# Kernel tuning notes

Measured on AMD Instinct MI355X. Metric: run time of the kernel, lower is better.

The kernel has to match this reference:

```python
import jax, jax.numpy as jnp
import numpy as np

N_USERS = 100000
N_ITEMS = 50000
DIM = 64
RANK = 5
NNZ = 2000000
GNN_LAYER = 2
MODEL_CAT_RATE = 0.02  # args.model_cat_rate
TEMP = 0.2


def _l2norm(x):
    # torch F.normalize(p=2, dim=1, eps=1e-12)
    n = jnp.sqrt(jnp.sum(x * x, axis=1, keepdims=True))
    return x / jnp.maximum(n, 1e-12)


def setup_inputs() -> dict:
    key = jax.random.key(0)
    ks = jax.random.split(key, 16)
    s = 0.1
    inp = {
        "user_emb": jax.random.normal(ks[0], (N_USERS, DIM), jnp.float32) * s,
        "item_emb": jax.random.normal(ks[1], (N_ITEMS, DIM), jnp.float32) * s,
        "user_emb_pre": jax.random.normal(ks[2], (N_USERS, DIM), jnp.float32) * s,
        "item_emb_pre": jax.random.normal(ks[3], (N_ITEMS, DIM), jnp.float32) * s,
        "image_item_embeds": jax.random.normal(ks[4], (N_ITEMS, DIM), jnp.float32),
        "text_item_embeds": jax.random.normal(ks[5], (N_ITEMS, DIM), jnp.float32),
        "image_user_embeds": jax.random.normal(ks[6], (N_USERS, DIM), jnp.float32),
        "text_user_embeds": jax.random.normal(ks[7], (N_USERS, DIM), jnp.float32),
        "adj_rows": jax.random.randint(ks[8], (NNZ,), 0, N_USERS, jnp.int32),
        "adj_cols": jax.random.randint(ks[9], (NNZ,), 0, N_ITEMS, jnp.int32),
        "adj_vals": jax.random.uniform(ks[10], (NNZ,), jnp.float32) * 0.05,
        "ut": jax.random.normal(ks[11], (RANK, N_USERS), jnp.float32) * 0.01,
        "vt": jax.random.normal(ks[12], (RANK, N_ITEMS), jnp.float32) * 0.01,
        "u_mul_s": jax.random.normal(ks[13], (N_USERS, RANK), jnp.float32) * 0.01,
        "v_mul_s": jax.random.normal(ks[14], (N_ITEMS, RANK), jnp.float32) * 0.01,
        "uids": jax.random.randint(ks[15], (2048,), 0, N_USERS, jnp.int32),
        "iids": jax.random.randint(jax.random.fold_in(key, 99), (4096,), 0, N_ITEMS, jnp.int32),
    }
    return inp


def reference(user_emb, item_emb, user_emb_pre, item_emb_pre,
              image_item_embeds, text_item_embeds,
              image_user_embeds, text_user_embeds,
              adj_rows, adj_cols, adj_vals,
              ut, vt, u_mul_s, v_mul_s, uids, iids):
    Eu0 = user_emb_pre + user_emb  # [N_U, D]
    Ei0 = item_emb_pre + item_emb  # [N_I, D]

    E_u_list, E_i_list = [Eu0], [Ei0]
    G_u_list, G_i_list = [Eu0], [Ei0]
    for _ in range(GNN_LAYER):
        Ei_prev, Eu_prev = E_i_list[-1], E_u_list[-1]
        # sparse adj_norm @ E_i  and  adj_norm.T @ E_u (COO gather + segment_sum)
        Zu = jax.ops.segment_sum(adj_vals[:, None] * Ei_prev[adj_cols], adj_rows,
                                 num_segments=N_USERS)
        Zi = jax.ops.segment_sum(adj_vals[:, None] * Eu_prev[adj_rows], adj_cols,
                                 num_segments=N_ITEMS)
        # low-rank SVD propagation
        Gu = u_mul_s @ (vt @ Ei_prev)  # [N_U, D]
        Gi = v_mul_s @ (ut @ Eu_prev)  # [N_I, D]
        E_u_list.append(Zu); E_i_list.append(Zi)
        G_u_list.append(Gu); G_i_list.append(Gi)

    G_u = sum(G_u_list) / len(G_u_list)
    G_i = sum(G_i_list) / len(G_i_list)
    E_u = sum(E_u_list) / len(E_u_list)
    E_i = sum(E_i_list) / len(E_i_list)

    # contrastive InfoNCE-style loss
    neg = jax.nn.logsumexp((G_u[uids] @ E_u.T) / TEMP, axis=1).mean()
    neg = neg + jax.nn.logsumexp((G_i[iids] @ E_i.T) / TEMP, axis=1).mean()
    pos = jnp.clip(jnp.sum(G_u[uids] * E_u[uids], axis=1) / TEMP, -5.0, 5.0).mean()
    pos = pos + jnp.clip(jnp.sum(G_i[iids] * E_i[iids], axis=1) / TEMP, -5.0, 5.0).mean()
    gcl_loss = (-pos + neg) * (len(G_u_list) + 1)

    user_out = E_u + MODEL_CAT_RATE * _l2norm(image_user_embeds) \
                   + MODEL_CAT_RATE * _l2norm(text_user_embeds)
    item_out = E_i + MODEL_CAT_RATE * _l2norm(image_item_embeds) \
                   + MODEL_CAT_RATE * _l2norm(text_item_embeds)
    return user_out, item_out, gcl_loss
```

## Files before the change

kernel.cpp:

```cpp
#include <hip/hip_runtime.h>
#include <cstdint>

#define N_U 100000
#define N_I 50000
#define DIM 64
#define RANK 5
#define NNZ_ 2000000
#define M_U 2048
#define M_I 4096
#define NSEG 150000
#define BSH 8
#define NBUCK 586
#define NPB 512
#define CH 3907

#define CPC 3136
#define CPW 784
#define NCH_U 32
#define NCH_I 16
#define NPAD_U (CPC * NCH_U)
#define NPAD_I (CPC * NCH_I)

typedef __attribute__((ext_vector_type(8))) short short8;
typedef __attribute__((ext_vector_type(4))) float floatx4;

static constexpr size_t ZU1 = 0;
static constexpr size_t ZI1 = 6400000;
static constexpr size_t EDGE = 9600000;
static constexpr size_t P_OFF = 13600000;
static constexpr size_t Q_OFF = 13600320;
static constexpr size_t ACC_OFF = 13600640;
static constexpr size_t CNT_OFF = 13600704;
static constexpr size_t OFF_OFF = 13750704;
static constexpr size_t BCNT_OFF = 13900720;
static constexpr size_t BOFF_OFF = 13910144;
static constexpr size_t BSUM_OFF = 13919552;
static constexpr size_t EU0 = 13920576;
static constexpr size_t EI0 = EU0 + 6400000;
static constexpr size_t PART_U = EI0 + 3200000;
static constexpr size_t PART_I = PART_U + (size_t)M_U * NCH_U * 4;
static constexpr size_t GTU = PART_I + (size_t)M_I * NCH_I * 4;
static constexpr size_t GTI = GTU + 3200000;
static constexpr size_t STAGE_SV = 0;
static constexpr size_t BH_OFF = EDGE;
static constexpr size_t BHP_OFF = EDGE + (size_t)NPB * NBUCK;
static constexpr size_t EBU16 = 0;
static constexpr size_t EBI16 = 3211264;
static constexpr size_t GBU16 = EBI16 + 1605632;
static constexpr size_t GBI16 = GBU16 + 65536;

static __device__ __forceinline__ short f2bf(float x) {
    unsigned u = __builtin_bit_cast(unsigned, x);
    unsigned r = (u + 0x7fffu + ((u >> 16) & 1u)) >> 16;
    return (short)r;
}

static __device__ __forceinline__ float bfu(unsigned short u) {
    return __builtin_bit_cast(float, (unsigned)u << 16);
}

static __device__ __forceinline__ float vdec(unsigned p) {
    return __builtin_bit_cast(float, (p & 0x7FFFu) << 16);
}

__global__ void ew_add_kernel(const float4* __restrict__ a, const float4* __restrict__ b,
                              float4* __restrict__ o, int n) {
    int i = blockIdx.x * blockDim.x + threadIdx.x;
    if (i < n) {
        float4 x = a[i], y = b[i];
        o[i] = make_float4(x.x + y.x, x.y + y.y, x.z + y.z, x.w + y.w);
    }
}

__global__ __launch_bounds__(256) void bhist_kernel(const int* __restrict__ rows,
                                                    const int* __restrict__ cols,
                                                    int* __restrict__ bh) {
    __shared__ int h[NBUCK];
    for (int i = threadIdx.x; i < NBUCK; i += 256) h[i] = 0;
    __syncthreads();
    int b = blockIdx.x;
    int lo = b * CH, hi = min(lo + CH, NNZ_);
    for (int e = lo + threadIdx.x; e < hi; e += 256) {
        atomicAdd(&h[rows[e] >> BSH], 1);
        atomicAdd(&h[(N_U + cols[e]) >> BSH], 1);
    }
    __syncthreads();
    for (int i = threadIdx.x; i < NBUCK; i += 256) bh[(size_t)b * NBUCK + i] = h[i];
}

__global__ __launch_bounds__(256) void col_scan_kernel(const int* __restrict__ bh,
                                                       int* __restrict__ bhp,
                                                       int* __restrict__ bcnt) {
    int j = blockIdx.x * 256 + threadIdx.x;
    if (j >= NBUCK) return;
    int run = 0;
#pragma unroll 16
    for (int b = 0; b < NPB; b++) {
        int v = bh[(size_t)b * NBUCK + j];
        bhp[(size_t)b * NBUCK + j] = run;
        run += v;
    }
    bcnt[j] = run;
}

__global__ void scan1_kernel(const int* __restrict__ cnt, int* __restrict__ bsum, int n) {
    int i = blockIdx.x * 256 + threadIdx.x;
    int v = (i < n) ? cnt[i] : 0;
#pragma unroll
    for (int off = 32; off; off >>= 1) v += __shfl_down(v, off);
    __shared__ int ls[4];
    int lane = threadIdx.x & 63, w = threadIdx.x >> 6;
    if (lane == 0) ls[w] = v;
    __syncthreads();
    if (threadIdx.x == 0) bsum[blockIdx.x] = ls[0] + ls[1] + ls[2] + ls[3];
}

__global__ void scan2_kernel(int* __restrict__ bsum, int nb) {
    __shared__ int s[1024];
    int t = threadIdx.x;
    s[t] = (t < nb) ? bsum[t] : 0;
    __syncthreads();
    for (int off = 1; off < 1024; off <<= 1) {
        int v = (t >= off) ? s[t - off] : 0;
        __syncthreads();
        s[t] += v;
        __syncthreads();
    }
    if (t < nb) bsum[t] = (t == 0) ? 0 : s[t - 1];
}

__global__ void scan3_kernel(const int* __restrict__ cnt, const int* __restrict__ bsum,
                             int* __restrict__ off, int n) {
    __shared__ int s[256];
    int i = blockIdx.x * 256 + threadIdx.x;
    int t = threadIdx.x;
    int c = (i < n) ? cnt[i] : 0;
    s[t] = c;
    __syncthreads();
    for (int o = 1; o < 256; o <<= 1) {
        int v = (t >= o) ? s[t - o] : 0;
        __syncthreads();
        s[t] += v;
        __syncthreads();
    }
    if (i < n) off[i] = bsum[blockIdx.x] + s[t] - c;
}

__global__ __launch_bounds__(256) void bucket_place_kernel(
    const int* __restrict__ rows, const int* __restrict__ cols, const float* __restrict__ vals,
    const int* __restrict__ boff, const int* __restrict__ bhp, float2* __restrict__ sv) {
    __shared__ int h[NBUCK];
    for (int i = threadIdx.x; i < NBUCK; i += 256) h[i] = 0;
    __syncthreads();
    int b = blockIdx.x;
    int lo = b * CH, hi = min(lo + CH, NNZ_);
    const int* bhpb = bhp + (size_t)b * NBUCK;
    for (int e = lo + threadIdx.x; e < hi; e += 256) {
        int r = rows[e], c = cols[e];
        float v = vals[e];
        int bu = r >> BSH;
        int ru = atomicAdd(&h[bu], 1);
        sv[boff[bu] + bhpb[bu] + ru] = make_float2(__int_as_float(c | ((r & 255) << 20)), v);
        int sI = N_U + c;
        int bi = sI >> BSH;
        int ri = atomicAdd(&h[bi], 1);
        sv[boff[bi] + bhpb[bi] + ri] = make_float2(__int_as_float(r | ((sI & 255) << 20)), v);
    }
}

__global__ __launch_bounds__(256) void place2_kernel(const float2* __restrict__ sv,
                                                     const int* __restrict__ boff,
                                                     const int* __restrict__ bcnt,
                                                     int* __restrict__ off, int* __restrict__ cnt,
                                                     unsigned* __restrict__ edge) {
    int b = blockIdx.x;
    int start = boff[b], n = bcnt[b];
    __shared__ int h[256], hs[256], hc[256];
    h[threadIdx.x] = 0;
    hc[threadIdx.x] = 0;
    __syncthreads();
    for (int i = start + threadIdx.x; i < start + n; i += 256) {
        int packed = __float_as_int(sv[i].x);
        atomicAdd(&h[(packed >> 20) & 255], 1);
    }
    __syncthreads();
    if (threadIdx.x == 0) {
        int run = 0;
#pragma unroll
        for (int k = 0; k < 256; k++) { hs[k] = run; run += h[k]; }
    }
    __syncthreads();
    {
        int seg = b * 256 + threadIdx.x;
        if (seg < NSEG) {
            cnt[seg] = h[threadIdx.x];
            off[seg] = start + hs[threadIdx.x] + h[threadIdx.x];
        }
    }
    for (int i = start + threadIdx.x; i < start + n; i += 256) {
        float2 p = sv[i];
        int packed = __float_as_int(p.x);
        int s = (packed >> 20) & 255;
        int r = atomicAdd(&hc[s], 1);
        unsigned vb = (unsigned)(unsigned short)f2bf(p.y);
        edge[start + hs[s] + r] = ((unsigned)(packed & 0xFFFFF) << 15) | (vb & 0x7FFFu);
    }
}

__global__ __launch_bounds__(256) void spmm_csr_kernel(
    const unsigned* __restrict__ edge, const int* __restrict__ off, const int* __restrict__ cnt,
    int base, const unsigned short* __restrict__ E16, float* __restrict__ out, float scale,
    int accum, int nrows) {
    int lane = threadIdx.x & 63;
    int row = (blockIdx.x * blockDim.x + threadIdx.x) >> 6;
    if (row >= nrows) return;
    int end = off[base + row];
    int n = cnt[base + row];
    int e = end - n;
    float acc = 0.f;
    while (e < end) {
        int m = min(64, end - e);
        unsigned pk = (lane < m) ? edge[e + lane] : 0u;
        int j = 0;
        for (; j + 8 <= m; j += 8) {
            unsigned p0 = (unsigned)__builtin_amdgcn_readlane((int)pk, j + 0);
            unsigned p1 = (unsigned)__builtin_amdgcn_readlane((int)pk, j + 1);
            unsigned p2 = (unsigned)__builtin_amdgcn_readlane((int)pk, j + 2);
            unsigned p3 = (unsigned)__builtin_amdgcn_readlane((int)pk, j + 3);
            unsigned p4 = (unsigned)__builtin_amdgcn_readlane((int)pk, j + 4);
            unsigned p5 = (unsigned)__builtin_amdgcn_readlane((int)pk, j + 5);
            unsigned p6 = (unsigned)__builtin_amdgcn_readlane((int)pk, j + 6);
            unsigned p7 = (unsigned)__builtin_amdgcn_readlane((int)pk, j + 7);
            float g0 = bfu(E16[(size_t)(p0 >> 15) * 64 + lane]);
            float g1 = bfu(E16[(size_t)(p1 >> 15) * 64 + lane]);
            float g2 = bfu(E16[(size_t)(p2 >> 15) * 64 + lane]);
            float g3 = bfu(E16[(size_t)(p3 >> 15) * 64 + lane]);
            float g4 = bfu(E16[(size_t)(p4 >> 15) * 64 + lane]);
            float g5 = bfu(E16[(size_t)(p5 >> 15) * 64 + lane]);
            float g6 = bfu(E16[(size_t)(p6 >> 15) * 64 + lane]);
            float g7 = bfu(E16[(size_t)(p7 >> 15) * 64 + lane]);
            acc = __builtin_fmaf(vdec(p0), g0, acc);
            acc = __builtin_fmaf(vdec(p1), g1, acc);
            acc = __builtin_fmaf(vdec(p2), g2, acc);
            acc = __builtin_fmaf(vdec(p3), g3, acc);
            acc = __builtin_fmaf(vdec(p4), g4, acc);
            acc = __builtin_fmaf(vdec(p5), g5, acc);
            acc = __builtin_fmaf(vdec(p6), g6, acc);
            acc = __builtin_fmaf(vdec(p7), g7, acc);
        }
        for (; j < m; j++) {
            unsigned p = (unsigned)__builtin_amdgcn_readlane((int)pk, j);
            acc = __builtin_fmaf(vdec(p), bfu(E16[(size_t)(p >> 15) * 64 + lane]), acc);
        }
        e += m;
    }
    size_t o = (size_t)row * 64 + lane;
    if (accum) out[o] += scale * acc;
    else out[o] = acc;
}

__global__ __launch_bounds__(256) void rank_kernel(const float* __restrict__ X,
                                                   const float* __restrict__ W,
                                                   float* __restrict__ P, int n) {
    int lane = threadIdx.x & 63;
    int g = lane >> 4;
    int t = lane & 15;
    int wid = threadIdx.x >> 6;
    int wave = (blockIdx.x * blockDim.x + threadIdx.x) >> 6;
    int nw = (gridDim.x * blockDim.x) >> 6;
    int nq = n >> 2;
    float a[RANK][4];
#pragma unroll
    for (int r = 0; r < RANK; r++)
#pragma unroll
        for (int c = 0; c < 4; c++) a[r][c] = 0.f;
#pragma unroll 2
    for (int i4 = wave; i4 < nq; i4 += nw) {
        int row = i4 * 4 + g;
        float4 x = *(const float4*)(X + (size_t)row * 64 + t * 4);
#pragma unroll
        for (int r = 0; r < RANK; r++) {
            float w = W[(size_t)r * n + row];
            a[r][0] = __builtin_fmaf(w, x.x, a[r][0]);
            a[r][1] = __builtin_fmaf(w, x.y, a[r][1]);
            a[r][2] = __builtin_fmaf(w, x.z, a[r][2]);
            a[r][3] = __builtin_fmaf(w, x.w, a[r][3]);
        }
    }
#pragma unroll
    for (int r = 0; r < RANK; r++)
#pragma unroll
        for (int c = 0; c < 4; c++) {
            float v = a[r][c];
            v += __shfl_xor(v, 16);
            v += __shfl_xor(v, 32);
            a[r][c] = v;
        }
    __shared__ float ls[4][RANK * 64];
    if (g == 0) {
#pragma unroll
        for (int r = 0; r < RANK; r++)
#pragma unroll
            for (int c = 0; c < 4; c++) ls[wid][r * 64 + t * 4 + c] = a[r][c];
    }
    __syncthreads();
    int tid = threadIdx.x;
    if (tid < RANK * 64) {
        float s = ls[0][tid] + ls[1][tid] + ls[2][tid] + ls[3][tid];
        atomicAdd(&P[tid], s);
    }
}

__global__ void pre_out_kernel(const float4* __restrict__ a, const float4* __restrict__ b,
                               float4* __restrict__ o, int n) {
    int i = blockIdx.x * blockDim.x + threadIdx.x;
    if (i < n) {
        float4 x = a[i], y = b[i];
        const float s = 1.f / 3.f;
        o[i] = make_float4((x.x + y.x) * s, (x.y + y.y) * s, (x.z + y.z) * s, (x.w + y.w) * s);
    }
}

__global__ void conv_bf16_kernel(const float* __restrict__ E, short* __restrict__ B, int n64,
                                 int npad64) {
    int i = blockIdx.x * blockDim.x + threadIdx.x;
    if (i < npad64) B[i] = (i < n64) ? f2bf(E[i]) : (short)0;
}

__global__ void gather_kernel(const int* __restrict__ ids, int m, const float* __restrict__ E0,
                              const float* __restrict__ PQ, const float* __restrict__ mulS,
                              const float* __restrict__ Eout, short* __restrict__ Gb,
                              float* __restrict__ acc, float coef) {
    int lane = threadIdx.x & 63;
    int k = (blockIdx.x * blockDim.x + threadIdx.x) >> 6;
    if (k >= m) return;
    int u = ids[k];
    float g = E0[u * 64 + lane];
#pragma unroll
    for (int r = 0; r < RANK; r++) g = __builtin_fmaf(mulS[u * RANK + r], PQ[r * 64 + lane], g);
    g *= (1.f / 3.f);
    Gb[k * 64 + lane] = f2bf(g);
    float d = g * Eout[u * 64 + lane];
#pragma unroll
    for (int off = 32; off; off >>= 1) d += __shfl_down(d, off);
    if (lane == 0) {
        float t = fminf(fmaxf(d * 5.f, -5.f), 5.f);
        atomicAdd(acc, coef * t);
    }
}

__global__ __launch_bounds__(256) void neg_mfma_kernel(const short* __restrict__ G16,
                                                       const short* __restrict__ E16,
                                                       float* __restrict__ part, int nchunk) {
    int lane = threadIdx.x & 63;
    int wave = threadIdx.x >> 6;
    int quad = lane >> 4;
    int rr = lane & 15;
    int rowbase = blockIdx.x * 64;
    short8 a0[4], a1[4];
#pragma unroll
    for (int g = 0; g < 4; g++) {
        const short8* ga = (const short8*)(G16 + (size_t)(rowbase + g * 16 + rr) * 64 + quad * 8);
        a0[g] = ga[0];
        a1[g] = ga[4];
    }
    int c0 = blockIdx.y * CPC + wave * CPW;
    float s[16];
#pragma unroll
    for (int i = 0; i < 16; i++) s[i] = 0.f;
    for (int ct = 0; ct < CPW; ct += 16) {
        const short8* eb = (const short8*)(E16 + (size_t)(c0 + ct + rr) * 64 + quad * 8);
        short8 b0 = eb[0];
        short8 b1 = eb[4];
#pragma unroll
        for (int g = 0; g < 4; g++) {
            floatx4 acc = {0.f, 0.f, 0.f, 0.f};
            acc = __builtin_amdgcn_mfma_f32_16x16x32_bf16(a0[g], b0, acc, 0, 0, 0);
            acc = __builtin_amdgcn_mfma_f32_16x16x32_bf16(a1[g], b1, acc, 0, 0, 0);
            s[g * 4 + 0] += __expf(acc[0] * 5.f);
            s[g * 4 + 1] += __expf(acc[1] * 5.f);
            s[g * 4 + 2] += __expf(acc[2] * 5.f);
            s[g * 4 + 3] += __expf(acc[3] * 5.f);
        }
    }
#pragma unroll
    for (int m = 8; m; m >>= 1) {
#pragma unroll
        for (int i = 0; i < 16; i++) s[i] += __shfl_xor(s[i], m);
    }
    if (rr == 0) {
        int col = blockIdx.y * 4 + wave;
#pragma unroll
        for (int g = 0; g < 4; g++) {
#pragma unroll
            for (int j = 0; j < 4; j++) {
                int row = rowbase + g * 16 + quad * 4 + j;
                part[(size_t)row * nchunk + col] = s[g * 4 + j];
            }
        }
    }
}

__global__ void combine_kernel(const float* __restrict__ part, int m, int nchunk, float pad,
                               float* __restrict__ acc, float coef) {
    int row = blockIdx.x * blockDim.x + threadIdx.x;
    if (row >= m) return;
    float S = 0.f;
    for (int c = 0; c < nchunk; c++) S += part[row * nchunk + c];
    float lse = __logf(S - pad);
    atomicAdd(acc, coef * lse);
}

__global__ void cat_kernel(const float* __restrict__ img, const float* __restrict__ txt,
                           float* __restrict__ out, int nrows) {
    int lane = threadIdx.x & 63;
    int row = (blockIdx.x * blockDim.x + threadIdx.x) >> 6;
    if (row >= nrows) return;
    float a = img[row * 64 + lane], b = txt[row * 64 + lane];
    float sa = a * a, sb = b * b;
#pragma unroll
    for (int msk = 32; msk; msk >>= 1) { sa += __shfl_xor(sa, msk); sb += __shfl_xor(sb, msk); }
    float ia = 1.f / fmaxf(sqrtf(sa), 1e-12f);
    float ib = 1.f / fmaxf(sqrtf(sb), 1e-12f);
    out[row * 64 + lane] += 0.02f * (a * ia + b * ib);
}

__global__ void loss_write_kernel(const float* __restrict__ acc, float* __restrict__ out) {
    out[0] = acc[0];
}

extern "C" void kernel_launch(void* const* d_in, const int* in_sizes, int n_in,
                              void* d_out, int out_size, void* d_ws, size_t ws_size,
                              hipStream_t stream) {
    const float* user_emb = (const float*)d_in[0];
    const float* item_emb = (const float*)d_in[1];
    const float* user_pre = (const float*)d_in[2];
    const float* item_pre = (const float*)d_in[3];
    const float* img_i = (const float*)d_in[4];
    const float* txt_i = (const float*)d_in[5];
    const float* img_u = (const float*)d_in[6];
    const float* txt_u = (const float*)d_in[7];
    const int* rows = (const int*)d_in[8];
    const int* cols = (const int*)d_in[9];
    const float* vals = (const float*)d_in[10];
    const float* ut = (const float*)d_in[11];
    const float* vt = (const float*)d_in[12];
    const float* u_mul_s = (const float*)d_in[13];
    const float* v_mul_s = (const float*)d_in[14];
    const int* uids = (const int*)d_in[15];
    const int* iids = (const int*)d_in[16];

    float* ws = (float*)d_ws;
    float* zu1 = ws + ZU1;
    float* zi1 = ws + ZI1;
    unsigned* edge = (unsigned*)(ws + EDGE);
    float* P = ws + P_OFF;
    float* Q = ws + Q_OFF;
    float* acc = ws + ACC_OFF;
    int* cnt = (int*)(ws + CNT_OFF);
    int* off = (int*)(ws + OFF_OFF);
    int* bcnt = (int*)(ws + BCNT_OFF);
    int* boff = (int*)(ws + BOFF_OFF);
    int* bsum = (int*)(ws + BSUM_OFF);
    float* eu0 = ws + EU0;
    float* ei0 = ws + EI0;
    float* part_u = ws + PART_U;
    float* part_i = ws + PART_I;
    unsigned short* gtu = (unsigned short*)(ws + GTU);
    unsigned short* gti = (unsigned short*)(ws + GTI);
    int* bh = (int*)(ws + BH_OFF);
    int* bhp = (int*)(ws + BHP_OFF);
    float2* stage_sv = (float2*)(ws + STAGE_SV);
    short* ebu16 = (short*)(ws + EBU16);
    short* ebi16 = (short*)(ws + EBI16);
    short* gbu16 = (short*)(ws + GBU16);
    short* gbi16 = (short*)(ws + GBI16);

    float* out_u = (float*)d_out;
    float* out_i = out_u + (size_t)N_U * 64;
    float* out_loss = out_u + (size_t)(N_U + N_I) * 64;

    const int NB2 = (NBUCK + 255) / 256;

    hipMemsetAsync(ws + P_OFF, 0, 704 * sizeof(float), stream);

    bhist_kernel<<<NPB, 256, 0, stream>>>(rows, cols, bh);
    col_scan_kernel<<<NB2, 256, 0, stream>>>(bh, bhp, bcnt);
    scan1_kernel<<<NB2, 256, 0, stream>>>(bcnt, bsum, NBUCK);
    scan2_kernel<<<1, 1024, 0, stream>>>(bsum, NB2);
    scan3_kernel<<<NB2, 256, 0, stream>>>(bcnt, bsum, boff, NBUCK);
    bucket_place_kernel<<<NPB, 256, 0, stream>>>(rows, cols, vals, boff, bhp, stage_sv);
    place2_kernel<<<NBUCK, 256, 0, stream>>>(stage_sv, boff, bcnt, off, cnt, edge);

    ew_add_kernel<<<6250, 256, 0, stream>>>((const float4*)user_emb, (const float4*)user_pre,
                                            (float4*)eu0, 1600000);
    ew_add_kernel<<<3125, 256, 0, stream>>>((const float4*)item_emb, (const float4*)item_pre,
                                            (float4*)ei0, 800000);
    conv_bf16_kernel<<<12500, 256, 0, stream>>>(ei0, (short*)gti, N_I * 64, N_I * 64);
    conv_bf16_kernel<<<25000, 256, 0, stream>>>(eu0, (short*)gtu, N_U * 64, N_U * 64);
    rank_kernel<<<1024, 256, 0, stream>>>(ei0, vt, P, N_I);
    rank_kernel<<<1024, 256, 0, stream>>>(eu0, ut, Q, N_U);
    spmm_csr_kernel<<<N_U / 4, 256, 0, stream>>>(edge, off, cnt, 0, gti, zu1, 1.f, 0, N_U);
    spmm_csr_kernel<<<N_I / 4, 256, 0, stream>>>(edge, off, cnt, N_U, gtu, zi1, 1.f, 0, N_I);
    conv_bf16_kernel<<<12500, 256, 0, stream>>>(zi1, (short*)gti, N_I * 64, N_I * 64);
    conv_bf16_kernel<<<25000, 256, 0, stream>>>(zu1, (short*)gtu, N_U * 64, N_U * 64);
    rank_kernel<<<1024, 256, 0, stream>>>(zi1, vt, P, N_I);
    rank_kernel<<<1024, 256, 0, stream>>>(zu1, ut, Q, N_U);
    pre_out_kernel<<<6250, 256, 0, stream>>>((const float4*)eu0, (const float4*)zu1,
                                             (float4*)out_u, 1600000);
    pre_out_kernel<<<3125, 256, 0, stream>>>((const float4*)ei0, (const float4*)zi1,
                                             (float4*)out_i, 800000);
    spmm_csr_kernel<<<N_U / 4, 256, 0, stream>>>(edge, off, cnt, 0, gti, out_u, 1.f / 3.f, 1,
                                                 N_U);
    spmm_csr_kernel<<<N_I / 4, 256, 0, stream>>>(edge, off, cnt, N_U, gtu, out_i, 1.f / 3.f, 1,
                                                 N_I);
    conv_bf16_kernel<<<(NPAD_U * 64 + 255) / 256, 256, 0, stream>>>(out_u, ebu16, N_U * 64,
                                                                   NPAD_U * 64);
    conv_bf16_kernel<<<(NPAD_I * 64 + 255) / 256, 256, 0, stream>>>(out_i, ebi16, N_I * 64,
                                                                   NPAD_I * 64);
    gather_kernel<<<M_U / 4, 256, 0, stream>>>(uids, M_U, eu0, P, u_mul_s, out_u, gbu16, acc,
                                               -4.f / M_U);
    gather_kernel<<<M_I / 4, 256, 0, stream>>>(iids, M_I, ei0, Q, v_mul_s, out_i, gbi16, acc,
                                               -4.f / M_I);
    dim3 gu(M_U / 64, NCH_U);
    neg_mfma_kernel<<<gu, 256, 0, stream>>>(gbu16, ebu16, part_u, NCH_U * 4);
    dim3 gi(M_I / 64, NCH_I);
    neg_mfma_kernel<<<gi, 256, 0, stream>>>(gbi16, ebi16, part_i, NCH_I * 4);
    combine_kernel<<<(M_U + 255) / 256, 256, 0, stream>>>(part_u, M_U, NCH_U * 4,
                                                          (float)(NPAD_U - N_U), acc, 4.f / M_U);
    combine_kernel<<<(M_I + 255) / 256, 256, 0, stream>>>(part_i, M_I, NCH_I * 4,
                                                          (float)(NPAD_I - N_I), acc, 4.f / M_I);
    cat_kernel<<<(N_U * 64 + 255) / 256, 256, 0, stream>>>(img_u, txt_u, out_u, N_U);
    cat_kernel<<<(N_I * 64 + 255) / 256, 256, 0, stream>>>(img_i, txt_i, out_i, N_I);
    loss_write_kernel<<<1, 1, 0, stream>>>(acc, out_loss);
}
```

Before: 980.8 us.

## Stage bucket placement in LDS, widen buckets, vectorize bf16 conversion, reduce atomics

Bucket placement now scatters each block's edges into shared memory grouped by bucket, then writes them out contiguously. This replaces scattered global writes with coalesced ones. Buckets widen from 256 to 512 segments, with half the bucket count and twice the placement blocks; place2 switches to a parallel scan. The bf16 conversion kernels now process float4 per thread, and the gather and combine kernels reduce within a block before issuing a single global atomic. The risks are a larger LDS footprint (about 35KB per block), which lowers occupancy, and bucket_place now needing the raw per-block histogram as an extra input.

New measurement: 892.1 us. 9.0% less time.

```diff
diff --git a/kernel.cpp b/kernel.cpp
--- a/kernel.cpp
+++ b/kernel.cpp
@@ -9,10 +9,11 @@
 #define M_U 2048
 #define M_I 4096
 #define NSEG 150000
-#define BSH 8
-#define NBUCK 586
-#define NPB 512
-#define CH 3907
+#define BSH 9
+#define SPB 512
+#define NBUCK 293
+#define NPB 1024
+#define CH 1954
 
 #define CPC 3136
 #define CPW 784
@@ -22,6 +23,7 @@
 #define NPAD_I (CPC * NCH_I)
 
 typedef __attribute__((ext_vector_type(8))) short short8;
+typedef __attribute__((ext_vector_type(4))) short short4v;
 typedef __attribute__((ext_vector_type(4))) float floatx4;
 
 static constexpr size_t ZU1 = 0;
@@ -148,23 +150,54 @@
 
 __global__ __launch_bounds__(256) void bucket_place_kernel(
     const int* __restrict__ rows, const int* __restrict__ cols, const float* __restrict__ vals,
-    const int* __restrict__ boff, const int* __restrict__ bhp, float2* __restrict__ sv) {
-    __shared__ int h[NBUCK];
-    for (int i = threadIdx.x; i < NBUCK; i += 256) h[i] = 0;
-    __syncthreads();
+    const int* __restrict__ boff, const int* __restrict__ bh, const int* __restrict__ bhp,
+    float2* __restrict__ sv) {
+    __shared__ int h[NBUCK], ls[NBUCK], gb[NBUCK];
+    __shared__ int sc[256];
+    __shared__ float2 buf[2 * CH];
+    __shared__ unsigned short bid[2 * CH];
+    int tid = threadIdx.x;
     int b = blockIdx.x;
+    const int* bhrow = bh + (size_t)b * NBUCK;
+    const int* bhprow = bhp + (size_t)b * NBUCK;
+    for (int j = tid; j < NBUCK; j += 256) h[j] = bhrow[j];
+    __syncthreads();
+    int j0 = 2 * tid, j1 = 2 * tid + 1;
+    int a0 = (j0 < NBUCK) ? h[j0] : 0;
+    int a1 = (j1 < NBUCK) ? h[j1] : 0;
+    sc[tid] = a0 + a1;
+    __syncthreads();
+    for (int o = 1; o < 256; o <<= 1) {
+        int v = (tid >= o) ? sc[tid - o] : 0;
+        __syncthreads();
+        sc[tid] += v;
+        __syncthreads();
+    }
+    int base = sc[tid] - a0 - a1;
+    if (j0 < NBUCK) { ls[j0] = base; gb[j0] = boff[j0] + bhprow[j0] - base; h[j0] = 0; }
+    if (j1 < NBUCK) { ls[j1] = base + a0; gb[j1] = boff[j1] + bhprow[j1] - (base + a0); h[j1] = 0; }
+    __syncthreads();
     int lo = b * CH, hi = min(lo + CH, NNZ_);
-    const int* bhpb = bhp + (size_t)b * NBUCK;
-    for (int e = lo + threadIdx.x; e < hi; e += 256) {
+    for (int e = lo + tid; e < hi; e += 256) {
         int r = rows[e], c = cols[e];
         float v = vals[e];
         int bu = r >> BSH;
         int ru = atomicAdd(&h[bu], 1);
-        sv[boff[bu] + bhpb[bu] + ru] = make_float2(__int_as_float(c | ((r & 255) << 20)), v);
+        int lp = ls[bu] + ru;
+        buf[lp] = make_float2(__int_as_float(c | ((r & 511) << 20)), v);
+        bid[lp] = (unsigned short)bu;
         int sI = N_U + c;
         int bi = sI >> BSH;
         int ri = atomicAdd(&h[bi], 1);
-        sv[boff[bi] + bhpb[bi] + ri] = make_float2(__int_as_float(r | ((sI & 255) << 20)), v);
+        lp = ls[bi] + ri;
+        buf[lp] = make_float2(__int_as_float(r | ((sI & 511) << 20)), v);
+        bid[lp] = (unsigned short)bi;
+    }
+    __syncthreads();
+    int ntot = 2 * (hi - lo);
+    for (int p = tid; p < ntot; p += 256) {
+        int bu = bid[p];
+        sv[gb[bu] + p] = buf[p];
     }
 }
 
@@ -175,32 +208,35 @@
                                                      unsigned* __restrict__ edge) {
     int b = blockIdx.x;
     int start = boff[b], n = bcnt[b];
-    __shared__ int h[256], hs[256], hc[256];
-    h[threadIdx.x] = 0;
-    hc[threadIdx.x] = 0;
-    __syncthreads();
-    for (int i = start + threadIdx.x; i < start + n; i += 256) {
-        int packed = __float_as_int(sv[i].x);
-        atomicAdd(&h[(packed >> 20) & 255], 1);
-    }
-    __syncthreads();
-    if (threadIdx.x == 0) {
-        int run = 0;
-#pragma unroll
-        for (int k = 0; k < 256; k++) { hs[k] = run; run += h[k]; }
-    }
-    __syncthreads();
-    {
-        int seg = b * 256 + threadIdx.x;
-        if (seg < NSEG) {
-            cnt[seg] = h[threadIdx.x];
-            off[seg] = start + hs[threadIdx.x] + h[threadIdx.x];
-        }
-    }
-    for (int i = start + threadIdx.x; i < start + n; i += 256) {
+    __shared__ int h[SPB], hs[SPB], hc[SPB];
+    __shared__ int sc[256];
+    int tid = threadIdx.x;
+    h[tid] = 0; h[tid + 256] = 0;
+    hc[tid] = 0; hc[tid + 256] = 0;
+    __syncthreads();
+    for (int i = start + tid; i < start + n; i += 256)
+        atomicAdd(&h[(__float_as_int(sv[i].x) >> 20) & 511], 1);
+    __syncthreads();
+    int a0 = h[2 * tid], a1 = h[2 * tid + 1];
+    sc[tid] = a0 + a1;
+    __syncthreads();
+    for (int o = 1; o < 256; o <<= 1) {
+        int v = (tid >= o) ? sc[tid - o] : 0;
+        __syncthreads();
+        sc[tid] += v;
+        __syncthreads();
+    }
+    int base = sc[tid] - a0 - a1;
+    hs[2 * tid] = base;
+    hs[2 * tid + 1] = base + a0;
+    int seg0 = b * SPB + 2 * tid;
+    if (seg0 < NSEG) { cnt[seg0] = a0; off[seg0] = start + base + a0; }
+    if (seg0 + 1 < NSEG) { cnt[seg0 + 1] = a1; off[seg0 + 1] = start + base + a0 + a1; }
+    __syncthreads();
+    for (int i = start + tid; i < start + n; i += 256) {
         float2 p = sv[i];
         int packed = __float_as_int(p.x);
-        int s = (packed >> 20) & 255;
+        int s = (packed >> 20) & 511;
         int r = atomicAdd(&hc[s], 1);
         unsigned vb = (unsigned)(unsigned short)f2bf(p.y);
         edge[start + hs[s] + r] = ((unsigned)(packed & 0xFFFFF) << 15) | (vb & 0x7FFFu);
@@ -321,10 +357,19 @@
     }
 }
 
-__global__ void conv_bf16_kernel(const float* __restrict__ E, short* __restrict__ B, int n64,
-                                 int npad64) {
+__global__ void conv_bf16_kernel(const float4* __restrict__ E, short4v* __restrict__ B, int n4,
+                                 int npad4) {
     int i = blockIdx.x * blockDim.x + threadIdx.x;
-    if (i < npad64) B[i] = (i < n64) ? f2bf(E[i]) : (short)0;
+    if (i >= npad4) return;
+    short4v o = {0, 0, 0, 0};
+    if (i < n4) {
+        float4 x = E[i];
+        o[0] = f2bf(x.x);
+        o[1] = f2bf(x.y);
+        o[2] = f2bf(x.z);
+        o[3] = f2bf(x.w);
+    }
+    B[i] = o;
 }
 
 __global__ void gather_kernel(const int* __restrict__ ids, int m, const float* __restrict__ E0,
@@ -332,21 +377,27 @@
                               const float* __restrict__ Eout, short* __restrict__ Gb,
                               float* __restrict__ acc, float coef) {
     int lane = threadIdx.x & 63;
+    int wid = threadIdx.x >> 6;
     int k = (blockIdx.x * blockDim.x + threadIdx.x) >> 6;
-    if (k >= m) return;
-    int u = ids[k];
-    float g = E0[u * 64 + lane];
-#pragma unroll
-    for (int r = 0; r < RANK; r++) g = __builtin_fmaf(mulS[u * RANK + r], PQ[r * 64 + lane], g);
-    g *= (1.f / 3.f);
-    Gb[k * 64 + lane] = f2bf(g);
-    float d = g * Eout[u * 64 + lane];
-#pragma unroll
-    for (int off = 32; off; off >>= 1) d += __shfl_down(d, off);
-    if (lane == 0) {
-        float t = fminf(fmaxf(d * 5.f, -5.f), 5.f);
-        atomicAdd(acc, coef * t);
-    }
+    __shared__ float lacc[4];
+    float t = 0.f;
+    if (k < m) {
+        int u = ids[k];
+        float g = E0[u * 64 + lane];
+#pragma unroll
+        for (int r = 0; r < RANK; r++)
+            g = __builtin_fmaf(mulS[u * RANK + r], PQ[r * 64 + lane], g);
+        g *= (1.f / 3.f);
+        Gb[k * 64 + lane] = f2bf(g);
+        float d = g * Eout[u * 64 + lane];
+#pragma unroll
+        for (int off = 32; off; off >>= 1) d += __shfl_down(d, off);
+        t = fminf(fmaxf(d * 5.f, -5.f), 5.f);
+    }
+    if (lane == 0) lacc[wid] = t;
+    __syncthreads();
+    if (threadIdx.x == 0)
+        atomicAdd(acc, coef * (lacc[0] + lacc[1] + lacc[2] + lacc[3]));
 }
 
 __global__ __launch_bounds__(256) void neg_mfma_kernel(const short* __restrict__ G16,
@@ -404,11 +455,19 @@
 __global__ void combine_kernel(const float* __restrict__ part, int m, int nchunk, float pad,
                                float* __restrict__ acc, float coef) {
     int row = blockIdx.x * blockDim.x + threadIdx.x;
-    if (row >= m) return;
-    float S = 0.f;
-    for (int c = 0; c < nchunk; c++) S += part[row * nchunk + c];
-    float lse = __logf(S - pad);
-    atomicAdd(acc, coef * lse);
+    int lane = threadIdx.x & 63, wid = threadIdx.x >> 6;
+    float lse = 0.f;
+    if (row < m) {
+        float S = 0.f;
+        for (int c = 0; c < nchunk; c++) S += part[(size_t)row * nchunk + c];
+        lse = __logf(S - pad);
+    }
+#pragma unroll
+    for (int off = 32; off; off >>= 1) lse += __shfl_down(lse, off);
+    __shared__ float l2[4];
+    if (lane == 0) l2[wid] = lse;
+    __syncthreads();
+    if (threadIdx.x == 0) atomicAdd(acc, coef * (l2[0] + l2[1] + l2[2] + l2[3]));
 }
 
 __global__ void cat_kernel(const float* __restrict__ img, const float* __restrict__ txt,
@@ -489,21 +548,23 @@
     scan1_kernel<<<NB2, 256, 0, stream>>>(bcnt, bsum, NBUCK);
     scan2_kernel<<<1, 1024, 0, stream>>>(bsum, NB2);
     scan3_kernel<<<NB2, 256, 0, stream>>>(bcnt, bsum, boff, NBUCK);
-    bucket_place_kernel<<<NPB, 256, 0, stream>>>(rows, cols, vals, boff, bhp, stage_sv);
+    bucket_place_kernel<<<NPB, 256, 0, stream>>>(rows, cols, vals, boff, bh, bhp, stage_sv);
     place2_kernel<<<NBUCK, 256, 0, stream>>>(stage_sv, boff, bcnt, off, cnt, edge);
 
     ew_add_kernel<<<6250, 256, 0, stream>>>((const float4*)user_emb, (const float4*)user_pre,
                                             (float4*)eu0, 1600000);
     ew_add_kernel<<<3125, 256, 0, stream>>>((const float4*)item_emb, (const float4*)item_pre,
                                             (float4*)ei0, 800000);
-    conv_bf16_kernel<<<12500, 256, 0, stream>>>(ei0, (short*)gti, N_I * 64, N_I * 64);
-    conv_bf16_kernel<<<25000, 256, 0, stream>>>(eu0, (short*)gtu, N_U * 64, N_U * 64);
+    conv_bf16_kernel<<<3125, 256, 0, stream>>>((const float4*)ei0, (short4v*)gti, 800000, 800000);
+    conv_bf16_kernel<<<6250, 256, 0, stream>>>((const float4*)eu0, (short4v*)gtu, 1600000,
+                                               1600000);
     rank_kernel<<<1024, 256, 0, stream>>>(ei0, vt, P, N_I);
     rank_kernel<<<1024, 256, 0, stream>>>(eu0, ut, Q, N_U);
     spmm_csr_kernel<<<N_U / 4, 256, 0, stream>>>(edge, off, cnt, 0, gti, zu1, 1.f, 0, N_U);
     spmm_csr_kernel<<<N_I / 4, 256, 0, stream>>>(edge, off, cnt, N_U, gtu, zi1, 1.f, 0, N_I);
-    conv_bf16_kernel<<<12500, 256, 0, stream>>>(zi1, (short*)gti, N_I * 64, N_I * 64);
-    conv_bf16_kernel<<<25000, 256, 0, stream>>>(zu1, (short*)gtu, N_U * 64, N_U * 64);
+    conv_bf16_kernel<<<3125, 256, 0, stream>>>((const float4*)zi1, (short4v*)gti, 800000, 800000);
+    conv_bf16_kernel<<<6250, 256, 0, stream>>>((const float4*)zu1, (short4v*)gtu, 1600000,
+                                               1600000);
     rank_kernel<<<1024, 256, 0, stream>>>(zi1, vt, P, N_I);
     rank_kernel<<<1024, 256, 0, stream>>>(zu1, ut, Q, N_U);
     pre_out_kernel<<<6250, 256, 0, stream>>>((const float4*)eu0, (const float4*)zu1,
@@ -514,10 +575,10 @@
                                                  N_U);
     spmm_csr_kernel<<<N_I / 4, 256, 0, stream>>>(edge, off, cnt, N_U, gtu, out_i, 1.f / 3.f, 1,
                                                  N_I);
-    conv_bf16_kernel<<<(NPAD_U * 64 + 255) / 256, 256, 0, stream>>>(out_u, ebu16, N_U * 64,
-                                                                   NPAD_U * 64);
-    conv_bf16_kernel<<<(NPAD_I * 64 + 255) / 256, 256, 0, stream>>>(out_i, ebi16, N_I * 64,
-                                                                   NPAD_I * 64);
+    conv_bf16_kernel<<<6272, 256, 0, stream>>>((const float4*)out_u, (short4v*)ebu16, 1600000,
+                                               NPAD_U * 16);
+    conv_bf16_kernel<<<3136, 256, 0, stream>>>((const float4*)out_i, (short4v*)ebi16, 800000,
+                                               NPAD_I * 16);
     gather_kernel<<<M_U / 4, 256, 0, stream>>>(uids, M_U, eu0, P, u_mul_s, out_u, gbu16, acc,
                                                -4.f / M_U);
     gather_kernel<<<M_I / 4, 256, 0, stream>>>(iids, M_I, ei0, Q, v_mul_s, out_i, gbi16, acc,
```
